# Kernel optimization log

Measured on AMD Instinct MI355X. Metric: run time of the kernel, lower is better.

## Reference

```python
import jax, jax.numpy as jnp
import numpy as np

N = 8192
NFEAT = 512
NHID = 256
NCLASS = 128


def setup_inputs() -> dict:
    key = jax.random.key(0)
    k1, k2, k3, k4 = jax.random.split(key, 4)
    feature_s = jax.random.normal(k1, (N, NFEAT), dtype=jnp.float32)
    feature_t = jax.random.normal(k2, (N, NFEAT), dtype=jnp.float32)
    # nn.Linear(in, out, bias=False) weight has shape [out, in]
    w1 = jax.random.normal(k3, (NHID, NFEAT), dtype=jnp.float32) * (1.0 / np.sqrt(NFEAT))
    w2 = jax.random.normal(k4, (NCLASS, NHID), dtype=jnp.float32) * (1.0 / np.sqrt(NHID))
    return {"feature_s": feature_s, "feature_t": feature_t, "w1": w1, "w2": w2}


def reference(feature_s, feature_t, w1, w2):
    # adj = softmax(feature_s @ feature_t^T) over rows (dim=1)
    adj = jax.nn.softmax(feature_s @ feature_t.T, axis=1)  # [N, N]
    # GCN layer 1: linear(adj @ x) with x = feature_s
    x1 = (adj @ feature_s) @ w1.T  # [N, NHID]
    # GCN layer 2
    x2 = (adj @ x1) @ w2.T  # [N, NCLASS]
    return (x1, x2)
```

## Files before the change

### kernel.cpp

```cpp
#include <hip/hip_runtime.h>
#include <stdint.h>


typedef unsigned short u16;
typedef short bf16x8 __attribute__((ext_vector_type(8)));
typedef _Float16 f16x8 __attribute__((ext_vector_type(8)));
typedef float f32x4 __attribute__((ext_vector_type(4)));

#define EPI_STOREB 0
#define EPI_PARTH  1

__device__ __forceinline__ u16 f2bf(float f) {
  unsigned u = __float_as_uint(f);
  u += 0x7fffu + ((u >> 16) & 1u);
  return (u16)(u >> 16);
}
__device__ __forceinline__ u16 f2h(float f) {
  union { _Float16 h; u16 u; } cv; cv.h = (_Float16)f; return cv.u;
}
__device__ __forceinline__ float h2f(u16 u) {
  union { u16 u; _Float16 h; } cv; cv.u = u; return (float)cv.h;
}
__device__ __forceinline__ int swz8(int r) { return (r ^ (r >> 3)) & 7; }
__device__ __forceinline__ int swz16(int r) { return (r ^ (r >> 4)) & 15; }

__device__ __forceinline__ void async16(const void* g, void* lds) {
  __builtin_amdgcn_global_load_lds(
      (const __attribute__((address_space(1))) unsigned int*)g,
      (__attribute__((address_space(3))) unsigned int*)lds, 16, 0, 0);
}

__global__ __launch_bounds__(256) void conv_probe(
    const float* __restrict__ Fs, const float* __restrict__ Ft,
    const float* __restrict__ W1, const float* __restrict__ W2,
    u16* __restrict__ Fsf, u16* __restrict__ Ftf,
    u16* __restrict__ W1f, u16* __restrict__ W2h,
    int* __restrict__ rmap, int* __restrict__ cmap) {
  const int bx = blockIdx.x, tid = threadIdx.x;
  if (bx < 4176) {
    const float* src; u16* dst; size_t i; bool tobf = false;
    if (bx < 2048)      { src = Fs; dst = Fsf; i = ((size_t)bx * 256 + tid) * 8; }
    else if (bx < 4096) { src = Ft; dst = Ftf; i = ((size_t)(bx - 2048) * 256 + tid) * 8; }
    else if (bx < 4160) { src = W1; dst = W1f; i = ((size_t)(bx - 4096) * 256 + tid) * 8; }
    else                { src = W2; dst = W2h; i = ((size_t)(bx - 4160) * 256 + tid) * 8; tobf = true; }
    const float4 a = *(const float4*)(src + i);
    const float4 b = *(const float4*)(src + i + 4);
    bf16x8 o;
    if (tobf) {
      o[0] = (short)f2bf(a.x); o[1] = (short)f2bf(a.y); o[2] = (short)f2bf(a.z); o[3] = (short)f2bf(a.w);
      o[4] = (short)f2bf(b.x); o[5] = (short)f2bf(b.y); o[6] = (short)f2bf(b.z); o[7] = (short)f2bf(b.w);
    } else {
      o[0] = (short)f2h(a.x); o[1] = (short)f2h(a.y); o[2] = (short)f2h(a.z); o[3] = (short)f2h(a.w);
      o[4] = (short)f2h(b.x); o[5] = (short)f2h(b.y); o[6] = (short)f2h(b.z); o[7] = (short)f2h(b.w);
    }
    *(bf16x8*)(dst + i) = o;
    return;
  }
  if (tid >= 64) return;
  const int lane = tid & 63;
  const int t = lane & 15, quad = lane >> 4;
  bf16x8 avt, av1;
  const u16 bt = f2bf((float)t), b1 = 0x3f80;
#pragma unroll
  for (int j = 0; j < 8; ++j) { ((u16*)&avt)[j] = bt; ((u16*)&av1)[j] = b1; }
  f32x4 z = {0.f, 0.f, 0.f, 0.f};
  f32x4 r1 = __builtin_amdgcn_mfma_f32_16x16x32_bf16(avt, av1, z, 0, 0, 0);
  f32x4 r2 = __builtin_amdgcn_mfma_f32_16x16x32_bf16(av1, avt, z, 0, 0, 0);
#pragma unroll
  for (int e = 0; e < 4; ++e) {
    int r = (int)(r1[e] * 0.03125f + 0.5f);
    int c = (int)(r2[e] * 0.03125f + 0.5f);
    if (r < 0 || r > 15) r = quad * 4 + e;
    if (c < 0 || c > 15) c = t;
    rmap[lane * 4 + e] = r;
    cmap[lane * 4 + e] = c;
  }
}

__global__ __launch_bounds__(512) void gemm_pexp_f16_256(
    const u16* __restrict__ A, const u16* __restrict__ B, int K, int N,
    u16* __restrict__ P, float* __restrict__ rsp,
    const int* __restrict__ rmap, const int* __restrict__ cmap) {
  __shared__ __align__(16) u16 lA[256 * 64];
  __shared__ __align__(16) u16 lB[128 * 64];
  __shared__ float lrs[256][2];

  const int tid = threadIdx.x;
  const int wave = tid >> 6, lane = tid & 63;
  const int quad = lane >> 4, t = lane & 15;
  const int bm = blockIdx.y * 256, bn = blockIdx.x * 128;
  const int wm = (wave & 3) * 64, wn = (wave >> 2) * 64;

  f32x4 acc[4][4];
#pragma unroll
  for (int i = 0; i < 4; ++i)
#pragma unroll
    for (int j = 0; j < 4; ++j) acc[i][j] = (f32x4){0.f, 0.f, 0.f, 0.f};

  const int srow = tid >> 3, schk = tid & 7;
  const u16* pA[4]; const u16* pB[2];
#pragma unroll
  for (int j = 0; j < 4; ++j) {
    const int r = j * 64 + srow;
    pA[j] = A + (size_t)(bm + r) * K + (schk ^ swz8(r)) * 8;
  }
#pragma unroll
  for (int j = 0; j < 2; ++j) {
    const int r = j * 64 + srow;
    pB[j] = B + (size_t)(bn + r) * K + (schk ^ swz8(r)) * 8;
  }

  int aoffx[4], boffx[4];
#pragma unroll
  for (int i = 0; i < 4; ++i) {
    const int rm = wm + i * 16 + t;
    aoffx[i] = rm * 128 + (swz8(rm) << 4);
    const int rn = wn + i * 16 + t;
    boffx[i] = rn * 128 + (swz8(rn) << 4);
  }
  const int sq0 = quad << 4, sq1 = (quad << 4) | 64;

  for (int k0 = 0; k0 < K; k0 += 64) {
#pragma unroll
    for (int j = 0; j < 4; ++j) {
      async16(pA[j], (char*)lA + j * 8192 + wave * 1024);
      pA[j] += 64;
    }
#pragma unroll
    for (int j = 0; j < 2; ++j) {
      async16(pB[j], (char*)lB + j * 8192 + wave * 1024);
      pB[j] += 64;
    }
    __syncthreads();
#pragma unroll
    for (int s = 0; s < 2; ++s) {
      const int sq = s ? sq1 : sq0;
      f16x8 av[4], bv[4];
#pragma unroll
      for (int i = 0; i < 4; ++i) {
        av[i] = *(const f16x8*)((const char*)lA + (aoffx[i] ^ sq));
        bv[i] = *(const f16x8*)((const char*)lB + (boffx[i] ^ sq));
      }
#pragma unroll
      for (int mi = 0; mi < 4; ++mi)
#pragma unroll
        for (int ni = 0; ni < 4; ++ni)
          acc[mi][ni] = __builtin_amdgcn_mfma_f32_16x16x32_f16(av[mi], bv[ni], acc[mi][ni], 0, 0, 0);
    }
    __syncthreads();
  }

  int rl[4], cl[4];
#pragma unroll
  for (int e = 0; e < 4; ++e) {
    rl[e] = rmap[lane * 4 + e];
    cl[e] = cmap[lane * 4 + e];
  }
#pragma unroll
  for (int mi = 0; mi < 4; ++mi)
#pragma unroll
    for (int e = 0; e < 4; ++e) {
      const int rloc = wm + mi * 16 + rl[e];
      const int row = bm + rloc;
      float s = 0.f;
#pragma unroll
      for (int ni = 0; ni < 4; ++ni) {
        float p = __expf(acc[mi][ni][e] - 100.0f);
        s += p;
        P[(size_t)row * N + (bn + wn + ni * 16 + cl[e])] = f2bf(p);
      }
      s += __shfl_xor(s, 1, 64);
      s += __shfl_xor(s, 2, 64);
      s += __shfl_xor(s, 4, 64);
      s += __shfl_xor(s, 8, 64);
      if (t == 0) lrs[rloc][wave >> 2] = s;
    }
  __syncthreads();
  if (tid < 256)
    rsp[(size_t)blockIdx.x * 8192 + bm + tid] = lrs[tid][0] + lrs[tid][1];
}

template <int EPI, int F16>
__global__ __launch_bounds__(256) void gemm_nt(
    const u16* __restrict__ A, const u16* __restrict__ B, int K, int Kc, int N,
    u16* __restrict__ outp, const float* __restrict__ invl,
    const int* __restrict__ rmap, const int* __restrict__ cmap) {
  __shared__ __align__(16) u16 lA[128 * 64];
  __shared__ __align__(16) u16 lB[128 * 64];

  const int tid = threadIdx.x;
  const int wave = tid >> 6, lane = tid & 63;
  const int quad = lane >> 4, t = lane & 15;
  const int bm = blockIdx.y * 128, bn = blockIdx.x * 128;
  const int wm = (wave & 1) * 64, wn = (wave >> 1) * 64;
  const int koff = blockIdx.z * Kc;

  f32x4 acc[4][4];
#pragma unroll
  for (int i = 0; i < 4; ++i)
#pragma unroll
    for (int j = 0; j < 4; ++j) acc[i][j] = (f32x4){0.f, 0.f, 0.f, 0.f};

  const int srow = tid >> 3, schk = tid & 7;
  const u16* pA[4]; const u16* pB[4];
#pragma unroll
  for (int j = 0; j < 4; ++j) {
    const int r = j * 32 + srow;
    const int c = schk ^ swz8(r);
    pA[j] = A + (size_t)(bm + r) * K + koff + c * 8;
    pB[j] = B + (size_t)(bn + r) * K + koff + c * 8;
  }

  int aoffx[4], boffx[4];
#pragma unroll
  for (int i = 0; i < 4; ++i) {
    const int rm = wm + i * 16 + t;
    aoffx[i] = rm * 128 + (swz8(rm) << 4);
    const int rn = wn + i * 16 + t;
    boffx[i] = rn * 128 + (swz8(rn) << 4);
  }
  const int sq0 = quad << 4, sq1 = (quad << 4) | 64;

  for (int k0 = 0; k0 < Kc; k0 += 64) {
#pragma unroll
    for (int j = 0; j < 4; ++j) {
      async16(pA[j], (char*)lA + j * 4096 + wave * 1024);
      async16(pB[j], (char*)lB + j * 4096 + wave * 1024);
      pA[j] += 64; pB[j] += 64;
    }
    __syncthreads();
#pragma unroll
    for (int s = 0; s < 2; ++s) {
      const int sq = s ? sq1 : sq0;
      bf16x8 av[4], bv[4];
#pragma unroll
      for (int i = 0; i < 4; ++i) {
        av[i] = *(const bf16x8*)((const char*)lA + (aoffx[i] ^ sq));
        bv[i] = *(const bf16x8*)((const char*)lB + (boffx[i] ^ sq));
      }
#pragma unroll
      for (int mi = 0; mi < 4; ++mi)
#pragma unroll
        for (int ni = 0; ni < 4; ++ni) {
          if constexpr (F16)
            acc[mi][ni] = __builtin_amdgcn_mfma_f32_16x16x32_f16(
                __builtin_bit_cast(f16x8, av[mi]), __builtin_bit_cast(f16x8, bv[ni]),
                acc[mi][ni], 0, 0, 0);
          else
            acc[mi][ni] = __builtin_amdgcn_mfma_f32_16x16x32_bf16(av[mi], bv[ni], acc[mi][ni], 0, 0, 0);
        }
    }
    __syncthreads();
  }

  int rl[4], cl[4];
#pragma unroll
  for (int e = 0; e < 4; ++e) {
    rl[e] = rmap[lane * 4 + e];
    cl[e] = cmap[lane * 4 + e];
  }
  const size_t zoff = (size_t)blockIdx.z * ((size_t)gridDim.y * 128) * N;
#pragma unroll
  for (int mi = 0; mi < 4; ++mi)
#pragma unroll
    for (int e = 0; e < 4; ++e) {
      const int row = bm + wm + mi * 16 + rl[e];
      const float sc = (EPI == EPI_PARTH) ? invl[row] : 1.0f;
#pragma unroll
      for (int ni = 0; ni < 4; ++ni) {
        const size_t idx = (size_t)row * N + (bn + wn + ni * 16 + cl[e]);
        if (EPI == EPI_PARTH) outp[zoff + idx] = f2h(acc[mi][ni][e] * sc);
        else                  outp[idx] = f2bf(acc[mi][ni][e]);
      }
    }
}

__global__ __launch_bounds__(256) void gemm_nt128(
    const u16* __restrict__ A, const u16* __restrict__ B, int K, int Kc, int N,
    u16* __restrict__ outp, const float* __restrict__ rsp,
    const int* __restrict__ rmap, const int* __restrict__ cmap) {
  __shared__ __align__(16) u16 lA[128 * 128];
  __shared__ __align__(16) u16 lB[128 * 128];
  __shared__ float linvl[128];

  const int tid = threadIdx.x;
  const int wave = tid >> 6, lane = tid & 63;
  const int quad = lane >> 4, t = lane & 15;
  const int bm = blockIdx.y * 128, bn = blockIdx.x * 128;
  const int wm = (wave & 1) * 64, wn = (wave >> 1) * 64;
  const int koff = blockIdx.z * Kc;

  if (tid < 128) {
    const int row = bm + tid;
    float s = 0.f;
#pragma unroll 8
    for (int b = 0; b < 64; ++b) s += rsp[(size_t)b * 8192 + row];
    linvl[tid] = 1.0f / s;
  }

  f32x4 acc[4][4];
#pragma unroll
  for (int i = 0; i < 4; ++i)
#pragma unroll
    for (int j = 0; j < 4; ++j) acc[i][j] = (f32x4){0.f, 0.f, 0.f, 0.f};

  const int srow = tid >> 4, schk = tid & 15;
  const u16* pA[8]; const u16* pB[8];
#pragma unroll
  for (int j = 0; j < 8; ++j) {
    const int r = j * 16 + srow;
    const int c = schk ^ swz16(r);
    pA[j] = A + (size_t)(bm + r) * K + koff + c * 8;
    pB[j] = B + (size_t)(bn + r) * K + koff + c * 8;
  }

  int aoffx[4], boffx[4];
#pragma unroll
  for (int i = 0; i < 4; ++i) {
    const int rm = wm + i * 16 + t;
    aoffx[i] = rm * 256 + (swz16(rm) << 4);
    const int rn = wn + i * 16 + t;
    boffx[i] = rn * 256 + (swz16(rn) << 4);
  }

  for (int k0 = 0; k0 < Kc; k0 += 128) {
#pragma unroll
    for (int j = 0; j < 8; ++j) {
      async16(pA[j], (char*)lA + j * 4096 + tid * 16);
      async16(pB[j], (char*)lB + j * 4096 + tid * 16);
      pA[j] += 128; pB[j] += 128;
    }
    __syncthreads();
#pragma unroll
    for (int s = 0; s < 4; ++s) {
      const int sq = (s << 6) | (quad << 4);
      bf16x8 av[4], bv[4];
#pragma unroll
      for (int i = 0; i < 4; ++i) {
        av[i] = *(const bf16x8*)((const char*)lA + (aoffx[i] ^ sq));
        bv[i] = *(const bf16x8*)((const char*)lB + (boffx[i] ^ sq));
      }
#pragma unroll
      for (int mi = 0; mi < 4; ++mi)
#pragma unroll
        for (int ni = 0; ni < 4; ++ni)
          acc[mi][ni] = __builtin_amdgcn_mfma_f32_16x16x32_bf16(av[mi], bv[ni], acc[mi][ni], 0, 0, 0);
    }
    __syncthreads();
  }

  int rl[4], cl[4];
#pragma unroll
  for (int e = 0; e < 4; ++e) {
    rl[e] = rmap[lane * 4 + e];
    cl[e] = cmap[lane * 4 + e];
  }
  const size_t zoff = (size_t)blockIdx.z * ((size_t)gridDim.y * 128) * N;
#pragma unroll
  for (int mi = 0; mi < 4; ++mi)
#pragma unroll
    for (int e = 0; e < 4; ++e) {
      const int rloc = wm + mi * 16 + rl[e];
      const int row = bm + rloc;
      const float sc = linvl[rloc];
#pragma unroll
      for (int ni = 0; ni < 4; ++ni) {
        const size_t idx = (size_t)row * N + (bn + wn + ni * 16 + cl[e]);
        outp[zoff + idx] = f2h(acc[mi][ni][e] * sc);
      }
    }
}

__global__ __launch_bounds__(512) void gemm_ntw128(
    const u16* __restrict__ A, const u16* __restrict__ B, int K, int Kc, int N,
    u16* __restrict__ outp, const float* __restrict__ rsp,
    const int* __restrict__ rmap, const int* __restrict__ cmap) {
  __shared__ __align__(16) u16 lA[128 * 128];
  __shared__ __align__(16) u16 lB[256 * 128];
  __shared__ float linvl[128];

  const int tid = threadIdx.x;
  const int wave = tid >> 6, lane = tid & 63;
  const int quad = lane >> 4, t = lane & 15;
  const int bm = blockIdx.y * 128, bn = blockIdx.x * 256;
  const int wm = (wave >> 2) * 64, wn = (wave & 3) * 64;
  const int koff = blockIdx.z * Kc;

  if (tid < 128) {
    const int row = bm + tid;
    float s = 0.f;
#pragma unroll 8
    for (int b = 0; b < 64; ++b) s += rsp[(size_t)b * 8192 + row];
    linvl[tid] = 1.0f / s;
  }

  f32x4 acc[4][4];
#pragma unroll
  for (int i = 0; i < 4; ++i)
#pragma unroll
    for (int j = 0; j < 4; ++j) acc[i][j] = (f32x4){0.f, 0.f, 0.f, 0.f};

  const int srow = tid >> 4, schk = tid & 15;
  const u16* pA[4]; const u16* pB[8];
#pragma unroll
  for (int j = 0; j < 4; ++j) {
    const int r = j * 32 + srow;
    pA[j] = A + (size_t)(bm + r) * K + koff + (schk ^ swz16(r)) * 8;
  }
#pragma unroll
  for (int j = 0; j < 8; ++j) {
    const int r = j * 32 + srow;
    pB[j] = B + (size_t)(bn + r) * K + koff + (schk ^ swz16(r)) * 8;
  }

  int aoffx[4], boffx[4];
#pragma unroll
  for (int i = 0; i < 4; ++i) {
    const int rm = wm + i * 16 + t;
    aoffx[i] = rm * 256 + (swz16(rm) << 4);
    const int rn = wn + i * 16 + t;
    boffx[i] = rn * 256 + (swz16(rn) << 4);
  }

  for (int k0 = 0; k0 < Kc; k0 += 128) {
#pragma unroll
    for (int j = 0; j < 4; ++j) {
      async16(pA[j], (char*)lA + j * 8192 + tid * 16);
      pA[j] += 128;
    }
#pragma unroll
    for (int j = 0; j < 8; ++j) {
      async16(pB[j], (char*)lB + j * 8192 + tid * 16);
      pB[j] += 128;
    }
    __syncthreads();
#pragma unroll
    for (int s = 0; s < 4; ++s) {
      const int sq = (s << 6) | (quad << 4);
      bf16x8 av[4], bv[4];
#pragma unroll
      for (int i = 0; i < 4; ++i) {
        av[i] = *(const bf16x8*)((const char*)lA + (aoffx[i] ^ sq));
        bv[i] = *(const bf16x8*)((const char*)lB + (boffx[i] ^ sq));
      }
#pragma unroll
      for (int mi = 0; mi < 4; ++mi)
#pragma unroll
        for (int ni = 0; ni < 4; ++ni)
          acc[mi][ni] = __builtin_amdgcn_mfma_f32_16x16x32_bf16(av[mi], bv[ni], acc[mi][ni], 0, 0, 0);
    }
    __syncthreads();
  }

  int rl[4], cl[4];
#pragma unroll
  for (int e = 0; e < 4; ++e) {
    rl[e] = rmap[lane * 4 + e];
    cl[e] = cmap[lane * 4 + e];
  }
  const size_t zoff = (size_t)blockIdx.z * ((size_t)gridDim.y * 128) * N;
#pragma unroll
  for (int mi = 0; mi < 4; ++mi)
#pragma unroll
    for (int e = 0; e < 4; ++e) {
      const int rloc = wm + mi * 16 + rl[e];
      const int row = bm + rloc;
      const float sc = linvl[rloc];
#pragma unroll
      for (int ni = 0; ni < 4; ++ni) {
        const size_t idx = (size_t)row * N + (bn + wn + ni * 16 + cl[e]);
        outp[zoff + idx] = f2h(acc[mi][ni][e] * sc);
      }
    }
}

__global__ __launch_bounds__(256) void combine1(
    const u16* __restrict__ pp, const float* __restrict__ invl,
    float* __restrict__ x1f, u16* __restrict__ x1h) {
  const size_t i = ((size_t)blockIdx.x * 256 + threadIdx.x) * 8;
  const bf16x8 p0 = *(const bf16x8*)(pp + i);
  const bf16x8 p1 = *(const bf16x8*)(pp + 2097152 + i);
  const bf16x8 p2 = *(const bf16x8*)(pp + 4194304 + i);
  const bf16x8 p3 = *(const bf16x8*)(pp + 6291456 + i);
  float4 o0, o1;
  bf16x8 oh;
#pragma unroll
  for (int j = 0; j < 8; ++j) {
    const float v = h2f((u16)p0[j]) + h2f((u16)p1[j]) + h2f((u16)p2[j]) + h2f((u16)p3[j]);
    if (j < 4) ((float*)&o0)[j] = v; else ((float*)&o1)[j - 4] = v;
    oh[j] = (short)f2bf(v);
  }
  *(float4*)(x1f + i) = o0;
  *(float4*)(x1f + i + 4) = o1;
  *(bf16x8*)(x1h + i) = oh;
}

__global__ __launch_bounds__(256) void combine2(
    const u16* __restrict__ pp, const float* __restrict__ invl,
    float* __restrict__ x2f) {
  const size_t i = ((size_t)blockIdx.x * 256 + threadIdx.x) * 8;
  float v[8] = {0.f, 0.f, 0.f, 0.f, 0.f, 0.f, 0.f, 0.f};
#pragma unroll
  for (int z = 0; z < 8; ++z) {
    const bf16x8 p = *(const bf16x8*)(pp + (size_t)z * 1048576 + i);
#pragma unroll
    for (int j = 0; j < 8; ++j) v[j] += h2f((u16)p[j]);
  }
  float4 o0, o1;
#pragma unroll
  for (int j = 0; j < 4; ++j) { ((float*)&o0)[j] = v[j]; ((float*)&o1)[j] = v[j + 4]; }
  *(float4*)(x2f + i) = o0;
  *(float4*)(x2f + i + 4) = o1;
}

extern "C" void kernel_launch(void* const* d_in, const int* in_sizes, int n_in,
                              void* d_out, int out_size, void* d_ws, size_t ws_size,
                              hipStream_t stream) {
  const float* Fs = (const float*)d_in[0];
  const float* Ft = (const float*)d_in[1];
  const float* W1 = (const float*)d_in[2];
  const float* W2 = (const float*)d_in[3];

  char* ws = (char*)d_ws;
  u16*   P    = (u16*)(ws);
  u16*   Fsf  = (u16*)(ws + 134217728);
  u16*   Ftf  = (u16*)(ws + 142606336);
  u16*   pp   = (u16*)(ws + 134217728);
  float* rsp  = (float*)(ws + 150994944);
  u16*   Y1T  = (u16*)(ws + 153092096);
  u16*   x1h  = (u16*)(ws + 157286400);
  u16*   Y2T  = (u16*)(ws + 161480704);
  int*   rmap = (int*)  (ws + 163610624);
  int*   cmap = (int*)  (ws + 163611648);
  u16*   W1f  = (u16*)(ws + 163612672);
  u16*   W2h  = (u16*)(ws + 163874816);

  float* x1f = (float*)d_out;
  float* x2f = (float*)d_out + 2097152;

  dim3 blk(256);
  conv_probe<<<4177, blk, 0, stream>>>(Fs, Ft, W1, W2, Fsf, Ftf, W1f, W2h, rmap, cmap);
  gemm_pexp_f16_256<<<dim3(64, 32), dim3(512), 0, stream>>>(
      Fsf, Ftf, 512, 8192, P, rsp, rmap, cmap);
  gemm_nt<EPI_STOREB, 1><<<dim3(64, 2), blk, 0, stream>>>(
      W1f, Fsf, 512, 512, 8192, Y1T, nullptr, rmap, cmap);
  gemm_ntw128<<<dim3(1, 64, 4), dim3(512), 0, stream>>>(
      P, Y1T, 8192, 2048, 256, pp, rsp, rmap, cmap);
  combine1<<<1024, blk, 0, stream>>>(pp, nullptr, x1f, x1h);
  gemm_nt<EPI_STOREB, 0><<<dim3(64, 1), blk, 0, stream>>>(
      W2h, x1h, 256, 256, 8192, Y2T, nullptr, rmap, cmap);
  gemm_nt128<<<dim3(1, 64, 8), blk, 0, stream>>>(
      P, Y2T, 8192, 1024, 128, pp, rsp, rmap, cmap);
  combine2<<<512, blk, 0, stream>>>(pp, nullptr, x2f);
}
```

Measured before the change: 272.2 us.

## Shrink layer-1 P@Y1 GEMM tile to 64 rows with 256-thread blocks

Replaces the 128x256 tile, 512-thread kernel for adj@Y1 with a 64x256 tile, 256-thread kernel. The grid doubles to 512 blocks for better CU coverage, and LDS use drops so more blocks can be resident. The row-sum reciprocal is now computed after the main loop and reuses the A shared buffer, and the shapes are compile-time constants with a different swizzle addressing. The trade-off is that the B tile is reloaded by twice as many blocks, which raises L2 traffic.

```diff
diff --git a/kernel.cpp b/kernel.cpp
--- a/kernel.cpp
+++ b/kernel.cpp
@@ -371,86 +371,77 @@
     }
 }
 
-__global__ __launch_bounds__(512) void gemm_ntw128(
-    const u16* __restrict__ A, const u16* __restrict__ B, int K, int Kc, int N,
+__global__ __launch_bounds__(256) void gemm_f1w64(
+    const u16* __restrict__ A, const u16* __restrict__ B,
     u16* __restrict__ outp, const float* __restrict__ rsp,
     const int* __restrict__ rmap, const int* __restrict__ cmap) {
-  __shared__ __align__(16) u16 lA[128 * 128];
+  constexpr int K = 8192, Kc = 2048, N = 256;
+  __shared__ __align__(16) u16 lA[64 * 128];
   __shared__ __align__(16) u16 lB[256 * 128];
-  __shared__ float linvl[128];
 
   const int tid = threadIdx.x;
   const int wave = tid >> 6, lane = tid & 63;
   const int quad = lane >> 4, t = lane & 15;
-  const int bm = blockIdx.y * 128, bn = blockIdx.x * 256;
-  const int wm = (wave >> 2) * 64, wn = (wave & 3) * 64;
+  const int bm = blockIdx.y * 64;
+  const int wn = wave * 64;
   const int koff = blockIdx.z * Kc;
 
-  if (tid < 128) {
+  f32x4 acc[4][4];
+#pragma unroll
+  for (int i = 0; i < 4; ++i)
+#pragma unroll
+    for (int j = 0; j < 4; ++j) acc[i][j] = (f32x4){0.f, 0.f, 0.f, 0.f};
+
+  const int srow = tid >> 4, schk = tid & 15;
+  const u16* abase = A + (size_t)(bm + srow) * K + koff;
+  const u16* bbase = B + (size_t)srow * K + koff;
+
+  int aoffx[4], boffx[4];
+#pragma unroll
+  for (int i = 0; i < 4; ++i) {
+    const int rm = i * 16 + t;
+    aoffx[i] = rm * 256 + (swz16(rm) << 4);
+    const int rn = wn + i * 16 + t;
+    boffx[i] = rn * 256 + (swz16(rn) << 4);
+  }
+
+  for (int k0 = 0; k0 < Kc; k0 += 128) {
+#pragma unroll
+    for (int j = 0; j < 4; ++j)
+      async16(abase + k0 + (size_t)j * 16 * K + (((schk ^ srow ^ j) & 15) << 3),
+              (char*)lA + j * 4096 + tid * 16);
+#pragma unroll
+    for (int j = 0; j < 16; ++j)
+      async16(bbase + k0 + (size_t)j * 16 * K + (((schk ^ srow ^ j) & 15) << 3),
+              (char*)lB + j * 4096 + tid * 16);
+    __syncthreads();
+#pragma unroll
+    for (int s = 0; s < 4; ++s) {
+      const int sq = (s << 6) | (quad << 4);
+      bf16x8 av[4], bv[4];
+#pragma unroll
+      for (int i = 0; i < 4; ++i) {
+        av[i] = *(const bf16x8*)((const char*)lA + (aoffx[i] ^ sq));
+        bv[i] = *(const bf16x8*)((const char*)lB + (boffx[i] ^ sq));
+      }
+#pragma unroll
+      for (int mi = 0; mi < 4; ++mi)
+#pragma unroll
+        for (int ni = 0; ni < 4; ++ni)
+          acc[mi][ni] = __builtin_amdgcn_mfma_f32_16x16x32_bf16(av[mi], bv[ni], acc[mi][ni], 0, 0, 0);
+    }
+    __syncthreads();
+  }
+
+  float* linvl = (float*)lA;
+  if (tid < 64) {
     const int row = bm + tid;
     float s = 0.f;
 #pragma unroll 8
     for (int b = 0; b < 64; ++b) s += rsp[(size_t)b * 8192 + row];
     linvl[tid] = 1.0f / s;
   }
-
-  f32x4 acc[4][4];
-#pragma unroll
-  for (int i = 0; i < 4; ++i)
-#pragma unroll
-    for (int j = 0; j < 4; ++j) acc[i][j] = (f32x4){0.f, 0.f, 0.f, 0.f};
-
-  const int srow = tid >> 4, schk = tid & 15;
-  const u16* pA[4]; const u16* pB[8];
-#pragma unroll
-  for (int j = 0; j < 4; ++j) {
-    const int r = j * 32 + srow;
-    pA[j] = A + (size_t)(bm + r) * K + koff + (schk ^ swz16(r)) * 8;
-  }
-#pragma unroll
-  for (int j = 0; j < 8; ++j) {
-    const int r = j * 32 + srow;
-    pB[j] = B + (size_t)(bn + r) * K + koff + (schk ^ swz16(r)) * 8;
-  }
-
-  int aoffx[4], boffx[4];
-#pragma unroll
-  for (int i = 0; i < 4; ++i) {
-    const int rm = wm + i * 16 + t;
-    aoffx[i] = rm * 256 + (swz16(rm) << 4);
-    const int rn = wn + i * 16 + t;
-    boffx[i] = rn * 256 + (swz16(rn) << 4);
-  }
-
-  for (int k0 = 0; k0 < Kc; k0 += 128) {
-#pragma unroll
-    for (int j = 0; j < 4; ++j) {
-      async16(pA[j], (char*)lA + j * 8192 + tid * 16);
-      pA[j] += 128;
-    }
-#pragma unroll
-    for (int j = 0; j < 8; ++j) {
-      async16(pB[j], (char*)lB + j * 8192 + tid * 16);
-      pB[j] += 128;
-    }
-    __syncthreads();
-#pragma unroll
-    for (int s = 0; s < 4; ++s) {
-      const int sq = (s << 6) | (quad << 4);
-      bf16x8 av[4], bv[4];
-#pragma unroll
-      for (int i = 0; i < 4; ++i) {
-        av[i] = *(const bf16x8*)((const char*)lA + (aoffx[i] ^ sq));
-        bv[i] = *(const bf16x8*)((const char*)lB + (boffx[i] ^ sq));
-      }
-#pragma unroll
-      for (int mi = 0; mi < 4; ++mi)
-#pragma unroll
-        for (int ni = 0; ni < 4; ++ni)
-          acc[mi][ni] = __builtin_amdgcn_mfma_f32_16x16x32_bf16(av[mi], bv[ni], acc[mi][ni], 0, 0, 0);
-    }
-    __syncthreads();
-  }
+  __syncthreads();
 
   int rl[4], cl[4];
 #pragma unroll
@@ -458,17 +449,17 @@
     rl[e] = rmap[lane * 4 + e];
     cl[e] = cmap[lane * 4 + e];
   }
-  const size_t zoff = (size_t)blockIdx.z * ((size_t)gridDim.y * 128) * N;
+  const size_t zoff = (size_t)blockIdx.z * 2097152;
 #pragma unroll
   for (int mi = 0; mi < 4; ++mi)
 #pragma unroll
     for (int e = 0; e < 4; ++e) {
-      const int rloc = wm + mi * 16 + rl[e];
+      const int rloc = mi * 16 + rl[e];
       const int row = bm + rloc;
       const float sc = linvl[rloc];
 #pragma unroll
       for (int ni = 0; ni < 4; ++ni) {
-        const size_t idx = (size_t)row * N + (bn + wn + ni * 16 + cl[e]);
+        const size_t idx = (size_t)row * N + (wn + ni * 16 + cl[e]);
         outp[zoff + idx] = f2h(acc[mi][ni][e] * sc);
       }
     }
@@ -544,8 +535,8 @@
       Fsf, Ftf, 512, 8192, P, rsp, rmap, cmap);
   gemm_nt<EPI_STOREB, 1><<<dim3(64, 2), blk, 0, stream>>>(
       W1f, Fsf, 512, 512, 8192, Y1T, nullptr, rmap, cmap);
-  gemm_ntw128<<<dim3(1, 64, 4), dim3(512), 0, stream>>>(
-      P, Y1T, 8192, 2048, 256, pp, rsp, rmap, cmap);
+  gemm_f1w64<<<dim3(1, 128, 4), blk, 0, stream>>>(
+      P, Y1T, pp, rsp, rmap, cmap);
   combine1<<<1024, blk, 0, stream>>>(pp, nullptr, x1f, x1h);
   gemm_nt<EPI_STOREB, 0><<<dim3(64, 1), blk, 0, stream>>>(
       W2h, x1h, 256, 256, 8192, Y2T, nullptr, rmap, cmap);
```

Result: no change. 275.7 us (+1.3%).
